# Kernel tuning notes

Hardware: AMD Instinct MI355X
Metric: run time of the kernel (lower is better)

The kernel has to match this reference:

```python
import jax, jax.numpy as jnp
import numpy as np

EMBED_DIM = 1024
HEADS = 16
HEAD_DIM = EMBED_DIM // HEADS
BATCH = 4
SEQ = 1024


def setup_inputs() -> dict:
    key = jax.random.key(0)
    ks = jax.random.split(key, 9)
    s = 1.0 / np.sqrt(HEAD_DIM)
    so = 1.0 / np.sqrt(EMBED_DIM)
    return {
        "values": jax.random.normal(ks[0], (BATCH, SEQ, EMBED_DIM), dtype=jnp.float32),
        "query": jax.random.normal(ks[1], (BATCH, SEQ, EMBED_DIM), dtype=jnp.float32),
        "key": jax.random.normal(ks[2], (BATCH, SEQ, EMBED_DIM), dtype=jnp.float32),
        "mask": jax.random.randint(ks[3], (BATCH, 1, SEQ, SEQ), 0, 2, dtype=jnp.int32),
        "Wv": jax.random.uniform(ks[4], (HEAD_DIM, HEAD_DIM), jnp.float32, -s, s),
        "Wk": jax.random.uniform(ks[5], (HEAD_DIM, HEAD_DIM), jnp.float32, -s, s),
        "Wq": jax.random.uniform(ks[6], (HEAD_DIM, HEAD_DIM), jnp.float32, -s, s),
        "Wo": jax.random.uniform(ks[7], (EMBED_DIM, EMBED_DIM), jnp.float32, -so, so),
        "bo": jax.random.uniform(ks[8], (EMBED_DIM,), jnp.float32, -so, so),
    }


def reference(values, query, key, mask, Wv, Wk, Wq, Wo, bo):
    N, Lq, E = query.shape
    Lk = key.shape[1]
    H, D = HEADS, HEAD_DIM
    # reshape to heads, then per-head shared linear projection (Linear(head_dim, head_dim), no bias)
    v = jnp.einsum('nlhd,ed->nlhe', values.reshape(N, Lk, H, D), Wv)
    k = jnp.einsum('nlhd,ed->nlhe', key.reshape(N, Lk, H, D), Wk)
    q = jnp.einsum('nlhd,ed->nlhe', query.reshape(N, Lq, H, D), Wq)
    # full [N,H,Q,K] scores, scaled by 1/sqrt(embed_dim) as in source
    sim = jnp.einsum('nqhd,nkhd->nhqk', q, k)
    sim = jnp.where(mask == 0, jnp.float32(-1e20), sim)
    attn = jax.nn.softmax(sim / jnp.sqrt(jnp.float32(E)), axis=3)
    out = jnp.einsum('nhqk,nkhd->nqhd', attn, v).reshape(N, Lq, H * D)
    return out @ Wo.T + bo
```

## Files before the change

### kernel.cpp

```cpp
#include <hip/hip_runtime.h>

#define SEQ 1024
#define HEADS 16
#define HD 64
#define EMB 1024

typedef short bf16x8 __attribute__((ext_vector_type(8)));
typedef float f32x4 __attribute__((ext_vector_type(4)));

static __device__ __forceinline__ unsigned cvtpk(float a, float b) {
  unsigned r;
  asm("v_cvt_pk_bf16_f32 %0, %1, %2" : "=v"(r) : "v"(a), "v"(b));
  return r;
}

static __device__ __forceinline__ void gload_lds16(const void* g, void* l) {
  __builtin_amdgcn_global_load_lds((const __attribute__((address_space(1))) unsigned int*)g,
                                   (__attribute__((address_space(3))) unsigned int*)l,
                                   16, 0, 0);
}

__global__ __launch_bounds__(256) void k_pp(const int* __restrict__ mask,
                                            const float* __restrict__ Wo,
                                            const float* __restrict__ Wv,
                                            const float* __restrict__ Wq,
                                            const float* __restrict__ Wk,
                                            const float* __restrict__ values,
                                            const float* __restrict__ query,
                                            const float* __restrict__ key,
                                            unsigned long long* __restrict__ mb,
                                            unsigned short* __restrict__ wob,
                                            unsigned short* __restrict__ vb,
                                            unsigned short* __restrict__ qb,
                                            unsigned short* __restrict__ kb) {
  __shared__ unsigned short Wl[64][64];
  const unsigned tid = threadIdx.x;
  const unsigned b = blockIdx.x;

  if (b < 3072) {
    const int lane = tid & 63, c = lane & 15, g = lane >> 4;
    const int wid = b * 4 + (tid >> 6);
    const int t = wid >> 12;
    const int rem = wid & 4095;
    const int n = rem >> 10, h = (rem >> 6) & 15, lb = rem & 63;

    const float* x; unsigned short* out;
    if (t == 0)      { x = values; out = vb; }
    else if (t == 1) { x = query;  out = qb; }
    else             { x = key;    out = kb; }
    const float* Wf = (t == 0) ? Wv : (t == 1) ? Wq : Wk;
    const float sc = (t == 1) ? 0.045084220027786356f : 1.0f;

    {
      const int row = tid >> 2, c0 = (tid & 3) * 16;
      const float4 f0 = *(const float4*)(Wf + row * 64 + c0);
      const float4 f1 = *(const float4*)(Wf + row * 64 + c0 + 4);
      const float4 f2 = *(const float4*)(Wf + row * 64 + c0 + 8);
      const float4 f3 = *(const float4*)(Wf + row * 64 + c0 + 12);
      uint4 u0, u1;
      u0.x = cvtpk(f0.x * sc, f0.y * sc); u0.y = cvtpk(f0.z * sc, f0.w * sc);
      u0.z = cvtpk(f1.x * sc, f1.y * sc); u0.w = cvtpk(f1.z * sc, f1.w * sc);
      u1.x = cvtpk(f2.x * sc, f2.y * sc); u1.y = cvtpk(f2.z * sc, f2.w * sc);
      u1.z = cvtpk(f3.x * sc, f3.y * sc); u1.w = cvtpk(f3.z * sc, f3.w * sc);
      const int s0 = ((c0 >> 3) ^ (row & 7)) << 4;
      const int s1 = (((c0 >> 3) + 1) ^ (row & 7)) << 4;
      *(uint4*)((char*)&Wl[0][0] + row * 128 + s0) = u0;
      *(uint4*)((char*)&Wl[0][0] + row * 128 + s1) = u1;
    }
    __syncthreads();

    bf16x8 bfr[4][2];
    #pragma unroll
    for (int cb = 0; cb < 4; ++cb) {
      const int row = cb * 16 + c;
      #pragma unroll
      for (int ks = 0; ks < 2; ++ks)
        bfr[cb][ks] = *(const bf16x8*)((char*)&Wl[0][0] + row * 128 +
                                       (((ks * 4 + g) ^ (c & 7)) << 4));
    }

    bf16x8 a[2];
    const float* xr = x + ((size_t)n * SEQ + lb * 16 + c) * EMB + h * HD;
    #pragma unroll
    for (int ks = 0; ks < 2; ++ks) {
      const float4 f0 = *(const float4*)(xr + ks * 32 + g * 8);
      const float4 f1 = *(const float4*)(xr + ks * 32 + g * 8 + 4);
      uint4 u;
      u.x = cvtpk(f0.x, f0.y); u.y = cvtpk(f0.z, f0.w);
      u.z = cvtpk(f1.x, f1.y); u.w = cvtpk(f1.z, f1.w);
      a[ks] = __builtin_bit_cast(bf16x8, u);
    }

    f32x4 acc[4] = {};
    #pragma unroll
    for (int cb = 0; cb < 4; ++cb)
      #pragma unroll
      for (int ks = 0; ks < 2; ++ks)
        acc[cb] = __builtin_amdgcn_mfma_f32_16x16x32_bf16(a[ks], bfr[cb][ks], acc[cb], 0, 0, 0);

    if (t == 0) {
      unsigned short* vt = out + (size_t)(n * HEADS + h) * (HD * SEQ);
      const int key0 = lb * 16 + 4 * g;
      #pragma unroll
      for (int cb = 0; cb < 4; ++cb) {
        const unsigned w0 = cvtpk(acc[cb][0], acc[cb][1]);
        const unsigned w1 = cvtpk(acc[cb][2], acc[cb][3]);
        *(uint2*)(vt + (size_t)(cb * 16 + c) * SEQ + key0) = make_uint2(w0, w1);
      }
    } else {
      unsigned short* op = out + ((size_t)(n * HEADS + h) * SEQ + lb * 16) * HD;
      #pragma unroll
      for (int r = 0; r < 4; ++r) {
        const unsigned w0 = cvtpk(acc[0][r], acc[1][r]);
        const unsigned w1 = cvtpk(acc[2][r], acc[3][r]);
        *(uint2*)(op + (4 * g + r) * HD + 4 * c) = make_uint2(w0, w1);
      }
    }
  } else if (b < 7168) {
    const unsigned lane = tid & 63u;
    const unsigned gwb = (b - 3072) * 16u + (tid >> 6) * 4u;
    #pragma unroll
    for (int it = 0; it < 4; ++it) {
      const unsigned gw = gwb + it;
      const int v = mask[(size_t)gw * 64u + lane];
      const unsigned long long bits = __ballot(v != 0);
      if (lane == 0) {
        const unsigned n = gw >> 14, qrow = (gw >> 4) & 1023u, ktile = gw & 15u;
        mb[((size_t)n * 16 + ktile) * 1024 + qrow] = bits;
      }
    }
  } else {
    const unsigned gid = (b - 7168) * 256u + tid;
    const unsigned e = gid >> 8, rem = gid & 255u;
    const unsigned blk = rem >> 4, cc = rem & 15u;
    const float* src = Wo + (size_t)e * 1024 + blk * 64 + cc;
    const unsigned w0 = cvtpk(src[0], src[16]);
    const unsigned w1 = cvtpk(src[32], src[48]);
    *(uint2*)(wob + (size_t)gid * 4) = make_uint2(w0, w1);
  }
}

__global__ __launch_bounds__(256, 4) void k_attn(const unsigned short* __restrict__ qb,
                                                 const unsigned short* __restrict__ kb,
                                                 const unsigned short* __restrict__ vb,
                                                 const unsigned long long* __restrict__ mb,
                                                 unsigned short* __restrict__ ob) {
  const int tid = threadIdx.x;
  const int w = tid >> 6, lane = tid & 63;
  const int c = lane & 15, g = lane >> 4;
  const int bid = blockIdx.x;
  const int nh = bid & 63, q64 = bid >> 6;
  const int n = nh >> 4, h = nh & 15;
  const int qlo = q64 * 64 + w * 16;

  __shared__ unsigned short Ks[2][64][64];
  __shared__ unsigned short Vs[2][64][64];
  __shared__ unsigned long long Ml[16][64];

  char* const Kb0 = (char*)&Ks[0][0][0];
  char* const Vb0 = (char*)&Vs[0][0][0];
  char* const Mb0 = (char*)&Ml[0][0];

  const size_t nhb = (size_t)(n * HEADS + h) * (SEQ * HD);
  const unsigned short* qp = qb + nhb;
  const char* kpB = (const char*)(kb + nhb);
  const char* vpB = (const char*)(vb + nhb);

  const char* kSrc[2]; const char* vSrc[2]; int ldsOff[2];
  #pragma unroll
  for (int i = 0; i < 2; ++i) {
    const int off = i * 4096 + tid * 16;
    const int row = off >> 7, slot = (off >> 4) & 7;
    const int krow = ((row >> 4) & 1) * 32 + ((row >> 5) & 1) * 4 +
                     ((row >> 2) & 3) * 8 + (row & 3);
    const int sw = (slot ^ (row & 7)) << 4;
    kSrc[i] = kpB + krow * 128 + sw;
    vSrc[i] = vpB + (size_t)row * 2048 + sw;
    ldsOff[i] = off;
  }

  bf16x8 qa[2];
  #pragma unroll
  for (int ks = 0; ks < 2; ++ks)
    qa[ks] = *(const bf16x8*)(qp + (size_t)(qlo + c) * HD + ks * 32 + g * 8);

  bf16x8 ones;
  #pragma unroll
  for (int j = 0; j < 8; ++j) ones[j] = (short)0x3F80;

  f32x4 o[4] = {};
  f32x4 lacc = {};

#define STAGEKV(dstK, dstV, kt_) do {                                   \
    _Pragma("unroll")                                                   \
    for (int i = 0; i < 2; ++i) {                                       \
      gload_lds16(kSrc[i] + (size_t)(kt_) * 8192, (dstK) + ldsOff[i]);  \
      gload_lds16(vSrc[i] + (kt_) * 128, (dstV) + ldsOff[i]);           \
    }                                                                   \
  } while (0)

  #pragma unroll
  for (int i = 0; i < 2; ++i) {
    const int moff = i * 4096 + tid * 16;
    const int mkt = moff >> 9;
    const char* msrc = (const char*)mb +
        ((size_t)(n * 16 + mkt) * 1024 + q64 * 64) * 8 + (moff & 511);
    gload_lds16(msrc, Mb0 + moff);
  }
  STAGEKV(Kb0, Vb0, 0);

  for (int kt = 0; kt < 16; ++kt) {
    const int cur = kt & 1;
    char* const Kc = Kb0 + cur * 8192;
    char* const Vc = Vb0 + cur * 8192;
    if (kt < 15) {
      STAGEKV(Kb0 + (cur ^ 1) * 8192, Vb0 + (cur ^ 1) * 8192, kt + 1);
      asm volatile("s_waitcnt vmcnt(4)" ::: "memory");
    } else {
      asm volatile("s_waitcnt vmcnt(0)" ::: "memory");
    }
    asm volatile("s_barrier" ::: "memory");

    const unsigned long long bits = Ml[kt][w * 16 + c];
    const unsigned blo = (unsigned)bits, bhi = (unsigned)(bits >> 32);

    bf16x8 kf[4][2];
    #pragma unroll
    for (int sub = 0; sub < 4; ++sub) {
      const int rho = sub * 16 + c;
      #pragma unroll
      for (int ks = 0; ks < 2; ++ks)
        kf[sub][ks] = *(const bf16x8*)(Kc + rho * 128 + (((ks * 4 + g) ^ (c & 7)) << 4));
    }

    f32x4 s[4];
    __builtin_amdgcn_s_setprio(1);
    #pragma unroll
    for (int sub = 0; sub < 4; ++sub) {
      f32x4 acc = {};
      acc = __builtin_amdgcn_mfma_f32_16x16x32_bf16(kf[sub][0], qa[0], acc, 0, 0, 0);
      acc = __builtin_amdgcn_mfma_f32_16x16x32_bf16(kf[sub][1], qa[1], acc, 0, 0, 0);
      s[sub] = acc;
    }
    __builtin_amdgcn_s_setprio(0);

    bf16x8 vf[4][2];
    #pragma unroll
    for (int db = 0; db < 4; ++db) {
      const int row = db * 16 + c;
      #pragma unroll
      for (int ks = 0; ks < 2; ++ks)
        vf[db][ks] = *(const bf16x8*)(Vc + row * 128 + (((ks * 4 + g) ^ (c & 7)) << 4));
    }

    unsigned pw[2][4];
    #pragma unroll
    for (int sub = 0; sub < 4; ++sub) {
      const unsigned x = ((sub & 1) ? bhi : blo) >> (8 * g + ((sub >> 1) << 2));
      const float p0 = (x & 1u) ? __builtin_exp2f(s[sub][0]) : 0.f;
      const float p1 = (x & 2u) ? __builtin_exp2f(s[sub][1]) : 0.f;
      const float p2 = (x & 4u) ? __builtin_exp2f(s[sub][2]) : 0.f;
      const float p3 = (x & 8u) ? __builtin_exp2f(s[sub][3]) : 0.f;
      pw[sub & 1][(sub >> 1) * 2 + 0] = cvtpk(p0, p1);
      pw[sub & 1][(sub >> 1) * 2 + 1] = cvtpk(p2, p3);
    }
    bf16x8 pa[2];
    pa[0] = __builtin_bit_cast(bf16x8, *(uint4*)&pw[0][0]);
    pa[1] = __builtin_bit_cast(bf16x8, *(uint4*)&pw[1][0]);

    __builtin_amdgcn_s_setprio(1);
    #pragma unroll
    for (int ks = 0; ks < 2; ++ks) {
      #pragma unroll
      for (int db = 0; db < 4; ++db)
        o[db] = __builtin_amdgcn_mfma_f32_16x16x32_bf16(pa[ks], vf[db][ks], o[db], 0, 0, 0);
      lacc = __builtin_amdgcn_mfma_f32_16x16x32_bf16(pa[ks], ones, lacc, 0, 0, 0);
    }
    __builtin_amdgcn_s_setprio(0);

    if (kt < 15) asm volatile("s_barrier" ::: "memory");
  }
#undef STAGEKV

  #pragma unroll
  for (int r = 0; r < 4; ++r) {
    const float inv = 1.0f / lacc[r];
    const unsigned w0 = cvtpk(o[0][r] * inv, o[1][r] * inv);
    const unsigned w1 = cvtpk(o[2][r] * inv, o[3][r] * inv);
    *(uint2*)(ob + ((size_t)n * SEQ + qlo + 4 * g + r) * EMB + h * 64 + 4 * c) =
        make_uint2(w0, w1);
  }
}

__global__ __launch_bounds__(256, 2) void k_gemm(const unsigned short* __restrict__ A,
                                                 const unsigned short* __restrict__ B,
                                                 const float* __restrict__ bo,
                                                 float* __restrict__ C) {
  const int tid = threadIdx.x;
  const int w = tid >> 6, lane = tid & 63;
  const int c = lane & 15, g = lane >> 4;
  const int bm = blockIdx.x & 31, bn = blockIdx.x >> 5;
  const int m0 = bm * 128, n0 = bn * 64;

  __shared__ unsigned short As[2][128][64];
  __shared__ unsigned short Bs[2][64][64];

  const char* aSrc[4]; int aOff[4];
  const char* bSrc[2]; int bOff[2];
  #pragma unroll
  for (int i = 0; i < 4; ++i) {
    const int off = i * 4096 + tid * 16;
    const int row = off >> 7, slot = (off >> 4) & 7;
    const int sw = (slot ^ (row & 7)) << 4;
    aSrc[i] = (const char*)A + (size_t)(m0 + row) * 2048 + sw;
    aOff[i] = off;
  }
  #pragma unroll
  for (int i = 0; i < 2; ++i) {
    const int off = i * 4096 + tid * 16;
    const int row = off >> 7, slot = (off >> 4) & 7;
    const int sw = (slot ^ (row & 7)) << 4;
    bSrc[i] = (const char*)B + (size_t)(n0 + row) * 2048 + sw;
    bOff[i] = off;
  }

  f32x4 acc[2][4] = {};

#define STAGE(buf, kt_) do {                                                  \
    _Pragma("unroll")                                                         \
    for (int i = 0; i < 4; ++i)                                               \
      gload_lds16(aSrc[i] + (kt_) * 128, (char*)&As[buf][0][0] + aOff[i]);    \
    _Pragma("unroll")                                                         \
    for (int i = 0; i < 2; ++i)                                               \
      gload_lds16(bSrc[i] + (kt_) * 128, (char*)&Bs[buf][0][0] + bOff[i]);    \
  } while (0)

  STAGE(0, 0);

  for (int kt = 0; kt < 16; ++kt) {
    const int cur = kt & 1;
    if (kt < 15) {
      STAGE(cur ^ 1, kt + 1);
      asm volatile("s_waitcnt vmcnt(6)" ::: "memory");
    } else {
      asm volatile("s_waitcnt vmcnt(0)" ::: "memory");
    }
    asm volatile("s_barrier" ::: "memory");

    #pragma unroll
    for (int ks = 0; ks < 2; ++ks) {
      bf16x8 af[2], bf_[4];
      #pragma unroll
      for (int i = 0; i < 2; ++i) {
        const int row = w * 32 + i * 16 + c;
        af[i] = *(const bf16x8*)((char*)&As[cur][0][0] + row * 128 +
                                 (((ks * 4 + g) ^ (c & 7)) << 4));
      }
      #pragma unroll
      for (int j = 0; j < 4; ++j) {
        const int row = j * 16 + c;
        bf_[j] = *(const bf16x8*)((char*)&Bs[cur][0][0] + row * 128 +
                                  (((ks * 4 + g) ^ (c & 7)) << 4));
      }
      __builtin_amdgcn_s_setprio(1);
      #pragma unroll
      for (int i = 0; i < 2; ++i)
        #pragma unroll
        for (int j = 0; j < 4; ++j)
          acc[i][j] = __builtin_amdgcn_mfma_f32_16x16x32_bf16(af[i], bf_[j], acc[i][j], 0, 0, 0);
      __builtin_amdgcn_s_setprio(0);
    }

    if (kt < 15) asm volatile("s_barrier" ::: "memory");
  }
#undef STAGE

  #pragma unroll
  for (int j = 0; j < 4; ++j) {
    const int col = n0 + j * 16 + c;
    const float bv = bo[col];
    #pragma unroll
    for (int i = 0; i < 2; ++i) {
      const int rowb = m0 + w * 32 + i * 16 + 4 * g;
      #pragma unroll
      for (int r = 0; r < 4; ++r)
        C[(size_t)(rowb + r) * 1024 + col] = acc[i][j][r] + bv;
    }
  }
}

extern "C" void kernel_launch(void* const* d_in, const int* in_sizes, int n_in,
                              void* d_out, int out_size, void* d_ws, size_t ws_size,
                              hipStream_t stream) {
  const float* values = (const float*)d_in[0];
  const float* query  = (const float*)d_in[1];
  const float* key    = (const float*)d_in[2];
  const int*   mask   = (const int*)d_in[3];
  const float* Wv     = (const float*)d_in[4];
  const float* Wk     = (const float*)d_in[5];
  const float* Wq     = (const float*)d_in[6];
  const float* Wo     = (const float*)d_in[7];
  const float* bo     = (const float*)d_in[8];
  float* out = (float*)d_out;

  char* ws = (char*)d_ws;
  unsigned short* qb = (unsigned short*)(ws);
  unsigned short* kb = (unsigned short*)(ws + (size_t)8 * 1024 * 1024);
  unsigned short* vb = (unsigned short*)(ws + (size_t)16 * 1024 * 1024);
  unsigned short* ob = (unsigned short*)(ws + (size_t)24 * 1024 * 1024);
  unsigned long long* mb = (unsigned long long*)(ws + (size_t)32 * 1024 * 1024);
  unsigned short* wob = (unsigned short*)(ws + (size_t)33 * 1024 * 1024);

  k_pp<<<8192, 256, 0, stream>>>(mask, Wo, Wv, Wq, Wk, values, query, key, mb, wob, vb, qb, kb);
  k_attn<<<1024, 256, 0, stream>>>(qb, kb, vb, mb, ob);
  k_gemm<<<512, 256, 0, stream>>>(ob, wob, bo, out);
}
```

Measured before the change: 77.56 us.

## Halve attention K/V tile to 32 keys and raise occupancy to 8 blocks

The attention kernel now walks 32 key tiles of 32 keys each instead of 16 tiles of 64. This halves the double-buffered K/V LDS footprint and raises the launch-bounds target from 4 to 8 blocks per CU. Mask bits are no longer staged through LDS; each lane reads its 32-bit mask word directly from global memory, prefetched one iteration ahead. The intent is more resident waves to hide latency, at the price of twice as many barriers and loop iterations, fewer MFMAs per sync, and tighter register limits that could cause spills.

```diff
diff --git a/kernel.cpp b/kernel.cpp
--- a/kernel.cpp
+++ b/kernel.cpp
@@ -140,7 +140,7 @@
   }
 }
 
-__global__ __launch_bounds__(256, 4) void k_attn(const unsigned short* __restrict__ qb,
+__global__ __launch_bounds__(256, 8) void k_attn(const unsigned short* __restrict__ qb,
                                                  const unsigned short* __restrict__ kb,
                                                  const unsigned short* __restrict__ vb,
                                                  const unsigned long long* __restrict__ mb,
@@ -153,134 +153,114 @@
   const int n = nh >> 4, h = nh & 15;
   const int qlo = q64 * 64 + w * 16;
 
-  __shared__ unsigned short Ks[2][64][64];
-  __shared__ unsigned short Vs[2][64][64];
-  __shared__ unsigned long long Ml[16][64];
+  __shared__ unsigned short Ks[2][32][64];
+  __shared__ unsigned short Vs[2][64][32];
 
   char* const Kb0 = (char*)&Ks[0][0][0];
   char* const Vb0 = (char*)&Vs[0][0][0];
-  char* const Mb0 = (char*)&Ml[0][0];
 
   const size_t nhb = (size_t)(n * HEADS + h) * (SEQ * HD);
   const unsigned short* qp = qb + nhb;
   const char* kpB = (const char*)(kb + nhb);
   const char* vpB = (const char*)(vb + nhb);
 
-  const char* kSrc[2]; const char* vSrc[2]; int ldsOff[2];
-  #pragma unroll
-  for (int i = 0; i < 2; ++i) {
-    const int off = i * 4096 + tid * 16;
-    const int row = off >> 7, slot = (off >> 4) & 7;
-    const int krow = ((row >> 4) & 1) * 32 + ((row >> 5) & 1) * 4 +
-                     ((row >> 2) & 3) * 8 + (row & 3);
-    const int sw = (slot ^ (row & 7)) << 4;
-    kSrc[i] = kpB + krow * 128 + sw;
-    vSrc[i] = vpB + (size_t)row * 2048 + sw;
-    ldsOff[i] = off;
-  }
-
   bf16x8 qa[2];
   #pragma unroll
   for (int ks = 0; ks < 2; ++ks)
     qa[ks] = *(const bf16x8*)(qp + (size_t)(qlo + c) * HD + ks * 32 + g * 8);
 
+  const char* kS; const char* vS; int sOf;
+  {
+    const int off = tid * 16;
+    sOf = off;
+    const int rho = off >> 7, sl = (off >> 4) & 7;
+    const int kap = 4 * (rho >> 4) + 8 * ((rho >> 2) & 3) + (rho & 3);
+    kS = kpB + (size_t)kap * 128 + ((sl ^ (rho & 7)) << 4);
+    const int d = off >> 6, sl2 = (off >> 4) & 3;
+    vS = vpB + (size_t)d * 2048 + ((sl2 ^ ((d >> 1) & 3)) << 4);
+  }
+
+  const char* const mgb = (const char*)mb + ((size_t)(n * 16) * 1024 + qlo + c) * 8;
+
   bf16x8 ones;
   #pragma unroll
   for (int j = 0; j < 8; ++j) ones[j] = (short)0x3F80;
 
   f32x4 o[4] = {};
   f32x4 lacc = {};
-
-#define STAGEKV(dstK, dstV, kt_) do {                                   \
-    _Pragma("unroll")                                                   \
-    for (int i = 0; i < 2; ++i) {                                       \
-      gload_lds16(kSrc[i] + (size_t)(kt_) * 8192, (dstK) + ldsOff[i]);  \
-      gload_lds16(vSrc[i] + (kt_) * 128, (dstV) + ldsOff[i]);           \
-    }                                                                   \
+  unsigned mcur, mnxt;
+
+#define STG(buf, t_) do {                                              \
+    gload_lds16(kS + (size_t)(t_) * 4096, Kb0 + (buf) * 4096 + sOf);   \
+    gload_lds16(vS + (t_) * 64, Vb0 + (buf) * 4096 + sOf);             \
   } while (0)
 
-  #pragma unroll
-  for (int i = 0; i < 2; ++i) {
-    const int moff = i * 4096 + tid * 16;
-    const int mkt = moff >> 9;
-    const char* msrc = (const char*)mb +
-        ((size_t)(n * 16 + mkt) * 1024 + q64 * 64) * 8 + (moff & 511);
-    gload_lds16(msrc, Mb0 + moff);
-  }
-  STAGEKV(Kb0, Vb0, 0);
-
-  for (int kt = 0; kt < 16; ++kt) {
-    const int cur = kt & 1;
-    char* const Kc = Kb0 + cur * 8192;
-    char* const Vc = Vb0 + cur * 8192;
-    if (kt < 15) {
-      STAGEKV(Kb0 + (cur ^ 1) * 8192, Vb0 + (cur ^ 1) * 8192, kt + 1);
-      asm volatile("s_waitcnt vmcnt(4)" ::: "memory");
+  mnxt = *(const unsigned*)(mgb);
+  STG(0, 0);
+
+  for (int t = 0; t < 32; ++t) {
+    const int cur = t & 1;
+    mcur = mnxt;
+
+    if (t < 31) {
+      mnxt = *(const unsigned*)(mgb + (size_t)((t + 1) >> 1) * 8192 + ((t + 1) & 1) * 4);
+      STG(cur ^ 1, t + 1);
+      asm volatile("s_waitcnt vmcnt(3)" ::: "memory");
     } else {
       asm volatile("s_waitcnt vmcnt(0)" ::: "memory");
     }
     asm volatile("s_barrier" ::: "memory");
 
-    const unsigned long long bits = Ml[kt][w * 16 + c];
-    const unsigned blo = (unsigned)bits, bhi = (unsigned)(bits >> 32);
-
-    bf16x8 kf[4][2];
-    #pragma unroll
-    for (int sub = 0; sub < 4; ++sub) {
+    char* const Kc = Kb0 + cur * 4096;
+    char* const Vc = Vb0 + cur * 4096;
+
+    bf16x8 kf[2][2];
+    #pragma unroll
+    for (int sub = 0; sub < 2; ++sub) {
       const int rho = sub * 16 + c;
       #pragma unroll
       for (int ks = 0; ks < 2; ++ks)
         kf[sub][ks] = *(const bf16x8*)(Kc + rho * 128 + (((ks * 4 + g) ^ (c & 7)) << 4));
     }
 
-    f32x4 s[4];
+    f32x4 s0 = {}, s1 = {};
     __builtin_amdgcn_s_setprio(1);
-    #pragma unroll
-    for (int sub = 0; sub < 4; ++sub) {
-      f32x4 acc = {};
-      acc = __builtin_amdgcn_mfma_f32_16x16x32_bf16(kf[sub][0], qa[0], acc, 0, 0, 0);
-      acc = __builtin_amdgcn_mfma_f32_16x16x32_bf16(kf[sub][1], qa[1], acc, 0, 0, 0);
-      s[sub] = acc;
-    }
+    s0 = __builtin_amdgcn_mfma_f32_16x16x32_bf16(kf[0][0], qa[0], s0, 0, 0, 0);
+    s0 = __builtin_amdgcn_mfma_f32_16x16x32_bf16(kf[0][1], qa[1], s0, 0, 0, 0);
+    s1 = __builtin_amdgcn_mfma_f32_16x16x32_bf16(kf[1][0], qa[0], s1, 0, 0, 0);
+    s1 = __builtin_amdgcn_mfma_f32_16x16x32_bf16(kf[1][1], qa[1], s1, 0, 0, 0);
     __builtin_amdgcn_s_setprio(0);
 
-    bf16x8 vf[4][2];
+    bf16x8 vf[4];
     #pragma unroll
     for (int db = 0; db < 4; ++db) {
-      const int row = db * 16 + c;
-      #pragma unroll
-      for (int ks = 0; ks < 2; ++ks)
-        vf[db][ks] = *(const bf16x8*)(Vc + row * 128 + (((ks * 4 + g) ^ (c & 7)) << 4));
-    }
-
-    unsigned pw[2][4];
-    #pragma unroll
-    for (int sub = 0; sub < 4; ++sub) {
-      const unsigned x = ((sub & 1) ? bhi : blo) >> (8 * g + ((sub >> 1) << 2));
-      const float p0 = (x & 1u) ? __builtin_exp2f(s[sub][0]) : 0.f;
-      const float p1 = (x & 2u) ? __builtin_exp2f(s[sub][1]) : 0.f;
-      const float p2 = (x & 4u) ? __builtin_exp2f(s[sub][2]) : 0.f;
-      const float p3 = (x & 8u) ? __builtin_exp2f(s[sub][3]) : 0.f;
-      pw[sub & 1][(sub >> 1) * 2 + 0] = cvtpk(p0, p1);
-      pw[sub & 1][(sub >> 1) * 2 + 1] = cvtpk(p2, p3);
-    }
-    bf16x8 pa[2];
-    pa[0] = __builtin_bit_cast(bf16x8, *(uint4*)&pw[0][0]);
-    pa[1] = __builtin_bit_cast(bf16x8, *(uint4*)&pw[1][0]);
+      const int d = db * 16 + c;
+      vf[db] = *(const bf16x8*)(Vc + d * 64 + ((g ^ ((c >> 1) & 3)) << 4));
+    }
+
+    const unsigned x = mcur >> (8 * g);
+    const float p0 = (x & 1u)   ? __builtin_exp2f(s0[0]) : 0.f;
+    const float p1 = (x & 2u)   ? __builtin_exp2f(s0[1]) : 0.f;
+    const float p2 = (x & 4u)   ? __builtin_exp2f(s0[2]) : 0.f;
+    const float p3 = (x & 8u)   ? __builtin_exp2f(s0[3]) : 0.f;
+    const float p4 = (x & 16u)  ? __builtin_exp2f(s1[0]) : 0.f;
+    const float p5 = (x & 32u)  ? __builtin_exp2f(s1[1]) : 0.f;
+    const float p6 = (x & 64u)  ? __builtin_exp2f(s1[2]) : 0.f;
+    const float p7 = (x & 128u) ? __builtin_exp2f(s1[3]) : 0.f;
+    const uint4 pu = make_uint4(cvtpk(p0, p1), cvtpk(p2, p3),
+                                cvtpk(p4, p5), cvtpk(p6, p7));
+    const bf16x8 pa = __builtin_bit_cast(bf16x8, pu);
 
     __builtin_amdgcn_s_setprio(1);
     #pragma unroll
-    for (int ks = 0; ks < 2; ++ks) {
-      #pragma unroll
-      for (int db = 0; db < 4; ++db)
-        o[db] = __builtin_amdgcn_mfma_f32_16x16x32_bf16(pa[ks], vf[db][ks], o[db], 0, 0, 0);
-      lacc = __builtin_amdgcn_mfma_f32_16x16x32_bf16(pa[ks], ones, lacc, 0, 0, 0);
-    }
+    for (int db = 0; db < 4; ++db)
+      o[db] = __builtin_amdgcn_mfma_f32_16x16x32_bf16(pa, vf[db], o[db], 0, 0, 0);
+    lacc = __builtin_amdgcn_mfma_f32_16x16x32_bf16(pa, ones, lacc, 0, 0, 0);
     __builtin_amdgcn_s_setprio(0);
 
-    if (kt < 15) asm volatile("s_barrier" ::: "memory");
-  }
-#undef STAGEKV
+    if (t < 31) asm volatile("s_barrier" ::: "memory");
+  }
+#undef STG
 
   #pragma unroll
   for (int r = 0; r < 4; ++r) {
```

After: 109.4 us. 41.0% more time.
